# Kernel optimization log

Hardware: AMD Instinct MI355X
Metric: run time of the kernel (lower is better)

The kernel has to match this reference:

```python
import jax, jax.numpy as jnp
import numpy as np

B, N, M = 256, 50, 100
FSD, FVD, LDIM, BBD, INTER, K = 300, 2048, 2048, 128, 512, 8


def _linear(x, W, b):
    return x @ W + b


def bb_process(bb, W, b):
    # bb: [..., 4] = (x1, y1, x2, y2)
    size = bb[..., 2:] - bb[..., :2]
    centre = bb[..., :2] + 0.5 * size
    area = size[..., 0:1] * size[..., 1:2]
    shp = size[..., 0:1] / (size[..., 1:2] + 1e-14)
    feats = jnp.concatenate([bb, size, centre, area, shp], axis=-1)  # [..., 10]
    return _linear(feats, W, b)


def setup_inputs() -> dict:
    key = jax.random.key(0)
    ks = jax.random.split(key, 20)
    def nrm(k, shape, s=0.02):
        return jax.random.normal(k, shape, jnp.float32) * s
    # valid boxes: x2>x1, y2>y1
    xy_s = jax.random.uniform(ks[0], (B, N, 2)); wh_s = jax.random.uniform(ks[1], (B, N, 2))
    ps = jnp.concatenate([xy_s, xy_s + wh_s], -1)
    xy_v = jax.random.uniform(ks[2], (B, M, 2)); wh_v = jax.random.uniform(ks[3], (B, M, 2))
    pv = jnp.concatenate([xy_v, xy_v + wh_v], -1)
    return {
        "l": jax.random.normal(ks[4], (B, LDIM), jnp.float32),
        "s": jax.random.normal(ks[5], (B, N, FSD), jnp.float32),
        "ps": ps,
        "mask_s": jax.random.randint(ks[6], (B,), 1, N + 1),
        "v_ori": jax.random.normal(ks[7], (B, M, FVD), jnp.float32),
        "pv": pv,
        "mask_v": jnp.full((B,), M, dtype=jnp.int32),
        "W_bb": nrm(ks[8], (10, BBD)), "b_bb": jnp.zeros((BBD,), jnp.float32),
        "W1": nrm(ks[9], (K, BBD, INTER), 0.05),
        "W2": nrm(ks[10], (K, BBD, INTER), 0.05),
        "W_fs": nrm(ks[11], (FSD + BBD, FVD + BBD)), "b_fs": jnp.zeros((FVD + BBD,), jnp.float32),
        "W_l2": nrm(ks[12], (LDIM, FVD + BBD)), "b_l2": jnp.zeros((FVD + BBD,), jnp.float32),
        "W_l3": nrm(ks[13], (LDIM, FVD + BBD)), "b_l3": jnp.zeros((FVD + BBD,), jnp.float32),
        "W_fv": nrm(ks[14], (FVD + BBD, FVD + BBD)), "b_fv": jnp.zeros((FVD + BBD,), jnp.float32),
        "W_o1": nrm(ks[15], (BBD + FVD, FSD)), "b_o1": jnp.zeros((FSD,), jnp.float32),
        "W_o2": nrm(ks[16], (BBD + FVD, FVD)), "b_o2": jnp.zeros((FVD,), jnp.float32),
        "epsilon": jax.random.normal(ks[17], (), jnp.float32),
    }


def reference(l, s, ps, mask_s, v_ori, pv, mask_v,
              W_bb, b_bb, W1, W2, W_fs, b_fs, W_l2, b_l2, W_l3, b_l3,
              W_fv, b_fv, W_o1, b_o1, W_o2, b_o2, epsilon):
    # eval mode: no dropout, no cooling noise. it=1 (only valid setting), penalty_ratio=10.
    s_bb = bb_process(ps, W_bb, b_bb)            # [B,N,BBD]
    v_bb = bb_process(pv, W_bb, b_bb)            # [B,M,BBD]
    v = jnp.concatenate([v_ori, v_bb], -1)       # [B,M,FVD+BBD]
    lq = l[:, None, :]                           # [B,1,LDIM]
    token_mask = jnp.arange(N)[None, :] < mask_s[:, None]   # [B,N] bool
    out_mask = token_mask[:, :, None].astype(s.dtype)        # [B,N,1]
    # K-head bilinear adjacency over bounding-box embeddings
    s_f = jnp.einsum('bnd,kdi->bkni', s_bb, W1)  # [B,K,N,INTER]
    v_f = jnp.einsum('bmd,kdi->bkmi', v_bb, W2)  # [B,K,M,INTER]
    adj = jnp.einsum('bkni,bkmi->bnm', s_f, v_f) / K  # mean over heads
    adj = jax.nn.softmax(adj, axis=2)
    # cooling: pow(relu(adj), 1/0.25) then renormalize
    adj = jax.nn.relu(adj) ** 4.0
    adj = adj / jnp.sum(adj, axis=-1, keepdims=True)
    adj = adj * out_mask                          # [B,N,M]
    # gated message sources
    prepared_s = jax.nn.relu(_linear(
        _linear(jnp.concatenate([s, s_bb], -1), W_fs, b_fs) * _linear(lq, W_l3, b_l3),
        W_o2, b_o2))                              # [B,N,FVD]
    prepared_v = jax.nn.relu(_linear(
        _linear(v, W_fv, b_fv) * jax.nn.softmax(_linear(lq, W_l2, b_l2), axis=-1),
        W_o1, b_o1))                              # [B,M,FSD]
    # masked matmul aggregation
    new_ele = jnp.einsum('bnm,bnd->bmd', adj, prepared_s)   # [B,M,FVD]
    v_out = epsilon * new_ele + v_ori
    s_out = jnp.concatenate([s, jnp.einsum('bnm,bmd->bnd', adj, prepared_v)], -1)  # [B,N,2*FSD]
    adj_inf = jnp.where(token_mask[:, :, None], adj, -jnp.inf)  # adj + inf_tmp
    fro = jnp.sum(jnp.linalg.norm(adj, axis=-1), axis=-1) / mask_s.astype(jnp.float32)
    loss = -jnp.sum(fro) / 10.0                   # att_loss / penalty_ratio
    return (s_out * out_mask, v_out, adj_inf, loss)
```

## Files before the change

### kernel.cpp

```cpp
#include <hip/hip_runtime.h>
#include <math.h>

#define B_ 256
#define N_ 50
#define M_ 100
#define FSD_ 300
#define FVD_ 2048
#define LDIM_ 2048
#define BBD_ 128
#define INTER_ 512
#define K_ 8
#define DFS_ 428
#define DV_ 2176
#define NEGBIG_ (-3.0e38f)

typedef __attribute__((ext_vector_type(8))) short bf16x8_t;
typedef __attribute__((ext_vector_type(4))) float f32x4_t;

__device__ __forceinline__ unsigned short f2bf(float x) {
  union { float f; unsigned int u; } c; c.f = x;
  unsigned int r = c.u + 0x7FFFu + ((c.u >> 16) & 1u);
  return (unsigned short)(r >> 16);
}

__device__ __forceinline__ void gload16(const void* g, void* l) {
  __builtin_amdgcn_global_load_lds(
      (const __attribute__((address_space(1))) void*)g,
      (__attribute__((address_space(3))) void*)l, 16, 0, 0);
}

__global__ __launch_bounds__(128) void bb_kernel(const float* __restrict__ pbox,
                                                 const float* __restrict__ W_bb,
                                                 const float* __restrict__ b_bb,
                                                 float* __restrict__ outbb) {
  int row = blockIdx.x;
  int o = threadIdx.x;
  const float* p = pbox + (size_t)row * 4;
  float x0 = p[0], y0 = p[1], x1 = p[2], y1 = p[3];
  float sx = x1 - x0, sy = y1 - y0;
  float f[10] = {x0, y0, x1, y1, sx, sy, x0 + 0.5f * sx, y0 + 0.5f * sy,
                 sx * sy, sx / (sy + 1e-14f)};
  float acc = b_bb[o];
#pragma unroll
  for (int i = 0; i < 10; i++) acc += f[i] * W_bb[i * BBD_ + o];
  outbb[(size_t)row * BBD_ + o] = acc;
}

__global__ __launch_bounds__(128) void wq_kernel(const float* __restrict__ W1,
                                                 const float* __restrict__ W2,
                                                 float* __restrict__ Wq) {
  int d = blockIdx.x, e = threadIdx.x;
  __shared__ float w1row[INTER_];
  float acc = 0.f;
  for (int k = 0; k < K_; k++) {
    __syncthreads();
    for (int i = e; i < INTER_; i += 128) w1row[i] = W1[((size_t)k * BBD_ + d) * INTER_ + i];
    __syncthreads();
    const float* w2 = W2 + ((size_t)k * BBD_ + e) * INTER_;
#pragma unroll 8
    for (int i = 0; i < INTER_; i++) acc += w1row[i] * w2[i];
  }
  Wq[d * BBD_ + e] = acc * (1.0f / K_);
}

__global__ __launch_bounds__(128) void t_kernel(const float* __restrict__ s_bb,
                                                const float* __restrict__ Wq,
                                                float* __restrict__ t) {
  int row = blockIdx.x, e = threadIdx.x;
  __shared__ float srow[BBD_];
  srow[e] = s_bb[(size_t)row * BBD_ + e];
  __syncthreads();
  float acc = 0;
#pragma unroll 8
  for (int d = 0; d < BBD_; d++) acc += srow[d] * Wq[d * BBD_ + e];
  t[(size_t)row * BBD_ + e] = acc;
}

__global__ __launch_bounds__(128) void adjdot_kernel(const float* __restrict__ t,
                                                     const float* __restrict__ v_bb,
                                                     float* __restrict__ adjw) {
  int row = blockIdx.x;
  int b = row / N_;
  int tid = threadIdx.x;
  __shared__ float tS[BBD_];
  tS[tid] = t[(size_t)row * BBD_ + tid];
  __syncthreads();
  if (tid < M_) {
    const float4* vr = (const float4*)(v_bb + ((size_t)b * M_ + tid) * BBD_);
    const float4* tr = (const float4*)tS;
    float acc = 0.f;
#pragma unroll 8
    for (int d4 = 0; d4 < BBD_ / 4; d4++) {
      float4 vv = vr[d4];
      float4 tt = tr[d4];
      acc += tt.x * vv.x + tt.y * vv.y + tt.z * vv.z + tt.w * vv.w;
    }
    adjw[(size_t)row * M_ + tid] = acc * 4.0f;
  }
}

__global__ __launch_bounds__(64) void adjsm_kernel(float* __restrict__ adjw,
                                                   const int* __restrict__ mask_s,
                                                   float* __restrict__ adj_inf,
                                                   float* __restrict__ lossbuf) {
  int row = blockIdx.x;
  int b = row / N_, n = row % N_;
  int tid = threadIdx.x;
  float* xr = adjw + (size_t)row * M_;
  int i1 = tid + 64;
  float v0 = xr[tid];
  float v1 = (i1 < M_) ? xr[i1] : -INFINITY;
  float mx = fmaxf(v0, v1);
#pragma unroll
  for (int off = 32; off > 0; off >>= 1) mx = fmaxf(mx, __shfl_xor(mx, off));
  float e0 = __expf(v0 - mx);
  float e1 = (i1 < M_) ? __expf(v1 - mx) : 0.f;
  float sm = e0 + e1;
#pragma unroll
  for (int off = 32; off > 0; off >>= 1) sm += __shfl_xor(sm, off);
  float inv = 1.0f / sm;
  int msk = mask_s[b];
  bool live = n < msk;
  float a0 = live ? e0 * inv : 0.f;
  float a1 = live ? e1 * inv : 0.f;
  xr[tid] = a0;
  adj_inf[(size_t)row * M_ + tid] = live ? a0 : NEGBIG_;
  if (i1 < M_) {
    xr[i1] = a1;
    adj_inf[(size_t)row * M_ + i1] = live ? a1 : NEGBIG_;
  }
  float n2 = a0 * a0 + a1 * a1;
#pragma unroll
  for (int off = 32; off > 0; off >>= 1) n2 += __shfl_xor(n2, off);
  if (tid == 0) lossbuf[row] = sqrtf(n2) / (float)msk;
}

__global__ __launch_bounds__(256) void lossred_kernel(const float* __restrict__ lossbuf,
                                                      float* __restrict__ loss) {
  int tid = threadIdx.x;
  float s = 0;
  for (int i = tid; i < B_ * N_; i += 256) s += lossbuf[i];
  __shared__ float red[4];
#pragma unroll
  for (int off = 32; off > 0; off >>= 1) s += __shfl_xor(s, off);
  if ((tid & 63) == 0) red[tid >> 6] = s;
  __syncthreads();
  if (tid == 0) loss[0] = -(red[0] + red[1] + red[2] + red[3]) / 10.0f;
}

__global__ __launch_bounds__(256) void softmax_kernel(float* __restrict__ g) {
  __shared__ float buf[DV_];
  __shared__ float red[4];
  __shared__ float bc;
  int b = blockIdx.x, tid = threadIdx.x;
  float* row = g + (size_t)b * DV_;
  float mx = -INFINITY;
  for (int i = tid; i < DV_; i += 256) {
    float v = row[i];
    buf[i] = v;
    mx = fmaxf(mx, v);
  }
#pragma unroll
  for (int off = 32; off > 0; off >>= 1) mx = fmaxf(mx, __shfl_xor(mx, off));
  if ((tid & 63) == 0) red[tid >> 6] = mx;
  __syncthreads();
  if (tid == 0) bc = fmaxf(fmaxf(red[0], red[1]), fmaxf(red[2], red[3]));
  __syncthreads();
  mx = bc;
  float sm = 0;
  for (int i = tid; i < DV_; i += 256) {
    float e = __expf(buf[i] - mx);
    buf[i] = e;
    sm += e;
  }
#pragma unroll
  for (int off = 32; off > 0; off >>= 1) sm += __shfl_xor(sm, off);
  if ((tid & 63) == 0) red[tid >> 6] = sm;
  __syncthreads();
  if (tid == 0) bc = red[0] + red[1] + red[2] + red[3];
  __syncthreads();
  float inv = 1.0f / bc;
  for (int i = tid; i < DV_; i += 256) row[i] = buf[i] * inv;
}

__global__ __launch_bounds__(256) void wtrans_kernel(const float* __restrict__ W,
                                                     unsigned short* __restrict__ Wt,
                                                     int K, int N, int Kpad) {
  __shared__ float tile[32][33];
  int n0 = blockIdx.x * 32, k0 = blockIdx.y * 32;
  int tj = threadIdx.x & 31, ti0 = threadIdx.x >> 5;
#pragma unroll
  for (int s = 0; s < 4; ++s) {
    int ki = k0 + ti0 + s * 8;
    int nj = n0 + tj;
    tile[ti0 + s * 8][tj] = (ki < K && nj < N) ? W[(size_t)ki * N + nj] : 0.f;
  }
  __syncthreads();
#pragma unroll
  for (int s = 0; s < 4; ++s) {
    int nloc = ti0 + s * 8;
    Wt[(size_t)(n0 + nloc) * Kpad + k0 + tj] = f2bf(tile[tj][nloc]);
  }
}

__global__ __launch_bounds__(256) void cat2bf_kernel(const float* __restrict__ A0, int ca,
                                                     const float* __restrict__ A1, int cb,
                                                     unsigned short* __restrict__ dst,
                                                     int cpad) {
  int row = blockIdx.y;
  int c4 = (blockIdx.x * 256 + threadIdx.x) * 4;
  if (c4 >= cpad) return;
  float4 v = make_float4(0.f, 0.f, 0.f, 0.f);
  if (c4 < ca)
    v = *(const float4*)(A0 + (size_t)row * ca + c4);
  else if (c4 < ca + cb)
    v = *(const float4*)(A1 + (size_t)row * cb + (c4 - ca));
  unsigned long long p = (unsigned long long)f2bf(v.x) |
                         ((unsigned long long)f2bf(v.y) << 16) |
                         ((unsigned long long)f2bf(v.z) << 32) |
                         ((unsigned long long)f2bf(v.w) << 48);
  *(unsigned long long*)(dst + (size_t)row * cpad + c4) = p;
}

template <int EPI, bool OBF>
__global__ __launch_bounds__(256) void mfma_gemm(
    const unsigned short* __restrict__ A, const unsigned short* __restrict__ Bt,
    const float* __restrict__ bias, const float* __restrict__ gate,
    void* __restrict__ Cout, int Kpad, int Ncols, int NStore, int ldc, int rows_per_b) {
  __shared__ unsigned short As[128 * 64];
  __shared__ unsigned short Bs[128 * 64];
  int tid = threadIdx.x;
  int wid = tid >> 6, lane = tid & 63;
  int wm = wid >> 1, wn = wid & 1;
  int lr = lane & 15, lh = lane >> 4;
  int row0 = blockIdx.y * 128, col0 = blockIdx.x * 128;

  f32x4_t acc[4][4];
#pragma unroll
  for (int m = 0; m < 4; ++m)
#pragma unroll
    for (int n = 0; n < 4; ++n) acc[m][n] = (f32x4_t){0.f, 0.f, 0.f, 0.f};

  int sr[4], sj[4];
#pragma unroll
  for (int c = 0; c < 4; ++c) {
    int b = ((c * 4 + wid) << 10) + lane * 16;
    sr[c] = b >> 7;
    sj[c] = ((b & 127) ^ ((sr[c] & 7) << 4)) >> 1;
  }

  int nK = Kpad >> 6;
  for (int kt = 0; kt < nK; ++kt) {
    int k0 = kt << 6;
#pragma unroll
    for (int c = 0; c < 4; ++c) {
      gload16(A + (size_t)(row0 + sr[c]) * Kpad + k0 + sj[c], &As[(c * 4 + wid) << 9]);
      gload16(Bt + (size_t)(col0 + sr[c]) * Kpad + k0 + sj[c], &Bs[(c * 4 + wid) << 9]);
    }
    __syncthreads();
    bf16x8_t af[4][2], bfr[4][2];
#pragma unroll
    for (int m = 0; m < 4; ++m) {
      int rl = wm * 64 + m * 16 + lr;
      int sw = (rl & 7) << 4;
#pragma unroll
      for (int kk = 0; kk < 2; ++kk) {
        int inner = ((kk * 64 + lh * 16) ^ sw) >> 1;
        af[m][kk] = *(const bf16x8_t*)&As[rl * 64 + inner];
      }
    }
#pragma unroll
    for (int n = 0; n < 4; ++n) {
      int nl = wn * 64 + n * 16 + lr;
      int sw = (nl & 7) << 4;
#pragma unroll
      for (int kk = 0; kk < 2; ++kk) {
        int inner = ((kk * 64 + lh * 16) ^ sw) >> 1;
        bfr[n][kk] = *(const bf16x8_t*)&Bs[nl * 64 + inner];
      }
    }
#pragma unroll
    for (int m = 0; m < 4; ++m)
#pragma unroll
      for (int n = 0; n < 4; ++n) {
        acc[m][n] = __builtin_amdgcn_mfma_f32_16x16x32_bf16(af[m][0], bfr[n][0], acc[m][n], 0, 0, 0);
        acc[m][n] = __builtin_amdgcn_mfma_f32_16x16x32_bf16(af[m][1], bfr[n][1], acc[m][n], 0, 0, 0);
      }
    __syncthreads();
  }

#pragma unroll
  for (int m = 0; m < 4; ++m) {
    int gr0 = row0 + wm * 64 + m * 16 + lh * 4;
#pragma unroll
    for (int n = 0; n < 4; ++n) {
      int gc = col0 + wn * 64 + n * 16 + lr;
      if (gc >= NStore) continue;
      float bv = bias[gc];
      f32x4_t v = acc[m][n];
#pragma unroll
      for (int i = 0; i < 4; ++i) {
        int gr = gr0 + i;
        float x = v[i] + bv;
        if constexpr (EPI == 1) x *= gate[(size_t)(gr / rows_per_b) * Ncols + gc];
        if constexpr (EPI == 2) x = fmaxf(x, 0.f);
        if constexpr (OBF)
          ((unsigned short*)Cout)[(size_t)gr * ldc + gc] = f2bf(x);
        else
          ((float*)Cout)[(size_t)gr * ldc + gc] = x;
      }
    }
  }
}

__global__ __launch_bounds__(128) void outv_kernel(const float* __restrict__ adjw,
                                                   const float* __restrict__ ps_prep,
                                                   const float* __restrict__ v_ori,
                                                   const float* __restrict__ eps_p,
                                                   float* __restrict__ v_out) {
  int b = blockIdx.x;
  int ch = blockIdx.y;
  int tid = threadIdx.x;
  __shared__ float psc[N_][128];
  __shared__ float adjs[N_ * M_];
  for (int i = tid; i < N_ * 128; i += 128) {
    int n = i >> 7, c = i & 127;
    psc[n][c] = ps_prep[((size_t)b * N_ + n) * FVD_ + ch * 128 + c];
  }
  for (int i = tid; i < N_ * M_; i += 128) adjs[i] = adjw[(size_t)b * N_ * M_ + i];
  __syncthreads();
  float eps = eps_p[0];
  int col4 = (tid & 31) * 4;
  int mbase = (tid >> 5) * 25;
  for (int mb = 0; mb < 25; mb += 5) {
    f32x4_t acc[5];
#pragma unroll
    for (int q = 0; q < 5; ++q) acc[q] = (f32x4_t){0.f, 0.f, 0.f, 0.f};
    const float* arow = adjs + mbase + mb;
#pragma unroll 2
    for (int n = 0; n < N_; ++n) {
      f32x4_t p = *(const f32x4_t*)&psc[n][col4];
#pragma unroll
      for (int q = 0; q < 5; ++q) acc[q] += arow[n * M_ + q] * p;
    }
#pragma unroll
    for (int q = 0; q < 5; ++q) {
      int m = mbase + mb + q;
      size_t base = ((size_t)b * M_ + m) * FVD_ + ch * 128 + col4;
      f32x4_t vo = *(const f32x4_t*)&v_ori[base];
      *(f32x4_t*)&v_out[base] = eps * acc[q] + vo;
    }
  }
}

__global__ __launch_bounds__(256) void outs_kernel(const float* __restrict__ s,
                                                   const float* __restrict__ adjw,
                                                   const float* __restrict__ pv_prep,
                                                   const int* __restrict__ mask_s,
                                                   float* __restrict__ s_out) {
  int b = blockIdx.x;
  int c0 = blockIdx.y * 64;
  int tid = threadIdx.x;
  __shared__ float pvc[M_ * 64];
  __shared__ float adjs[52 * M_];
  for (int i = tid; i < M_ * 64; i += 256) {
    int m = i >> 6, c = c0 + (i & 63);
    pvc[i] = (c < FSD_) ? pv_prep[((size_t)b * M_ + m) * FSD_ + c] : 0.f;
  }
  for (int i = tid; i < 52 * M_; i += 256)
    adjs[i] = (i < N_ * M_) ? adjw[(size_t)b * N_ * M_ + i] : 0.f;
  __syncthreads();
  int col = tid & 63, ngrp = tid >> 6;
  int msk = mask_s[b];
  float acc[13];
#pragma unroll
  for (int i = 0; i < 13; ++i) acc[i] = 0.f;
  for (int m = 0; m < M_; ++m) {
    float pv = pvc[m * 64 + col];
#pragma unroll
    for (int i = 0; i < 13; ++i) acc[i] += adjs[(ngrp * 13 + i) * M_ + m] * pv;
  }
  int gc = c0 + col;
  if (gc < FSD_) {
#pragma unroll
    for (int i = 0; i < 13; ++i) {
      int n = ngrp * 13 + i;
      if (n >= N_) break;
      size_t row = (size_t)b * N_ + n;
      bool live = n < msk;
      s_out[row * (2 * FSD_) + gc] = live ? s[row * FSD_ + gc] : 0.f;
      s_out[row * (2 * FSD_) + FSD_ + gc] = acc[i];
    }
  }
}

extern "C" void kernel_launch(void* const* d_in, const int* in_sizes, int n_in,
                              void* d_out, int out_size, void* d_ws, size_t ws_size,
                              hipStream_t stream) {
  (void)in_sizes; (void)n_in; (void)out_size; (void)ws_size;
  const float* l = (const float*)d_in[0];
  const float* s = (const float*)d_in[1];
  const float* ps_box = (const float*)d_in[2];
  const int* mask_s = (const int*)d_in[3];
  const float* v_ori = (const float*)d_in[4];
  const float* pv_box = (const float*)d_in[5];
  const float* W_bb = (const float*)d_in[7];
  const float* b_bb = (const float*)d_in[8];
  const float* W1 = (const float*)d_in[9];
  const float* W2 = (const float*)d_in[10];
  const float* W_fs = (const float*)d_in[11];
  const float* b_fs = (const float*)d_in[12];
  const float* W_l2 = (const float*)d_in[13];
  const float* b_l2 = (const float*)d_in[14];
  const float* W_l3 = (const float*)d_in[15];
  const float* b_l3 = (const float*)d_in[16];
  const float* W_fv = (const float*)d_in[17];
  const float* b_fv = (const float*)d_in[18];
  const float* W_o1 = (const float*)d_in[19];
  const float* b_o1 = (const float*)d_in[20];
  const float* W_o2 = (const float*)d_in[21];
  const float* b_o2 = (const float*)d_in[22];
  const float* eps = (const float*)d_in[23];

  float* ws = (float*)d_ws;
  float* s_bb = ws;
  float* v_bb = s_bb + 1638400;
  float* Wq = v_bb + 3276800;
  float* t = Wq + 16384;
  float* adjw = t + 1638400;
  float* lossbuf = adjw + 1280000;
  float* g3 = lossbuf + 12800;
  float* g2 = g3 + 557056;
  float* ps_prep = g2 + 557056;
  float* pv_prep = ps_prep + 26214400;
  unsigned short* bfb = (unsigned short*)(pv_prep + 7680000);
  unsigned short* R1 = bfb;
  unsigned short* R2 = R1 + 55705600;
  unsigned short* Wt_fs = R2 + 55705600;
  unsigned short* Wt_o2 = Wt_fs + 974848;
  unsigned short* Wt_fv = Wt_o2 + 4456448;
  unsigned short* Wt_o1 = Wt_fv + 4734976;
  unsigned short* Wt_l2 = Wt_o1 + 835584;
  unsigned short* Wt_l3 = Wt_l2 + 4456448;
  unsigned short* A_l = Wt_l3 + 4456448;
  unsigned short* A_fv = R1;
  unsigned short* A_fs = R1;
  unsigned short* h_bf = R1 + 8000000;
  unsigned short* y_bf = R2;

  float* out = (float*)d_out;
  float* o_sout = out;
  float* o_vout = out + 7680000;
  float* o_adjinf = out + 60108800;
  float* o_loss = out + 61388800;

  bb_kernel<<<B_ * N_, 128, 0, stream>>>(ps_box, W_bb, b_bb, s_bb);
  bb_kernel<<<B_ * M_, 128, 0, stream>>>(pv_box, W_bb, b_bb, v_bb);
  wq_kernel<<<BBD_, 128, 0, stream>>>(W1, W2, Wq);
  t_kernel<<<B_ * N_, 128, 0, stream>>>(s_bb, Wq, t);
  adjdot_kernel<<<B_ * N_, 128, 0, stream>>>(t, v_bb, adjw);
  adjsm_kernel<<<B_ * N_, 64, 0, stream>>>(adjw, mask_s, o_adjinf, lossbuf);
  lossred_kernel<<<1, 256, 0, stream>>>(lossbuf, o_loss);

  wtrans_kernel<<<dim3(68, 64), 256, 0, stream>>>(W_l3, Wt_l3, LDIM_, DV_, 2048);
  wtrans_kernel<<<dim3(68, 64), 256, 0, stream>>>(W_l2, Wt_l2, LDIM_, DV_, 2048);
  wtrans_kernel<<<dim3(68, 68), 256, 0, stream>>>(W_fv, Wt_fv, DV_, DV_, 2176);
  wtrans_kernel<<<dim3(12, 68), 256, 0, stream>>>(W_o1, Wt_o1, DV_, FSD_, 2176);
  wtrans_kernel<<<dim3(68, 14), 256, 0, stream>>>(W_fs, Wt_fs, DFS_, DV_, 448);
  wtrans_kernel<<<dim3(64, 68), 256, 0, stream>>>(W_o2, Wt_o2, DV_, FVD_, 2176);
  cat2bf_kernel<<<dim3(2, B_), 256, 0, stream>>>(l, LDIM_, nullptr, 0, A_l, 2048);

  mfma_gemm<0, false><<<dim3(17, 2), 256, 0, stream>>>(A_l, Wt_l3, b_l3, nullptr, g3,
                                                       2048, DV_, DV_, DV_, 1);
  mfma_gemm<0, false><<<dim3(17, 2), 256, 0, stream>>>(A_l, Wt_l2, b_l2, nullptr, g2,
                                                       2048, DV_, DV_, DV_, 1);
  softmax_kernel<<<B_, 256, 0, stream>>>(g2);

  cat2bf_kernel<<<dim3(3, B_ * M_), 256, 0, stream>>>(v_ori, FVD_, v_bb, BBD_, A_fv, 2176);
  mfma_gemm<1, true><<<dim3(17, 200), 256, 0, stream>>>(A_fv, Wt_fv, b_fv, g2, y_bf,
                                                        2176, DV_, DV_, DV_, M_);
  mfma_gemm<2, false><<<dim3(3, 200), 256, 0, stream>>>(y_bf, Wt_o1, b_o1, nullptr, pv_prep,
                                                        2176, DV_, FSD_, FSD_, 1);

  cat2bf_kernel<<<dim3(1, B_ * N_), 256, 0, stream>>>(s, FSD_, s_bb, BBD_, A_fs, 448);
  mfma_gemm<1, true><<<dim3(17, 100), 256, 0, stream>>>(A_fs, Wt_fs, b_fs, g3, h_bf,
                                                        448, DV_, DV_, DV_, N_);
  mfma_gemm<2, false><<<dim3(16, 100), 256, 0, stream>>>(h_bf, Wt_o2, b_o2, nullptr, ps_prep,
                                                         2176, FVD_, FVD_, FVD_, 1);

  outv_kernel<<<dim3(B_, 16), 128, 0, stream>>>(adjw, ps_prep, v_ori, eps, o_vout);
  outs_kernel<<<dim3(B_, 5), 256, 0, stream>>>(s, adjw, pv_prep, mask_s, o_sout);
}
```

Measured before the change: 1.792 ms.

## Double-buffer GEMM LDS tiles, remap workgroups across XCDs, merge query GEMMs

The MFMA GEMM now uses two LDS buffers so the global loads for the next K tile are issued while the current tile is computed, which halves the barriers per tile. Workgroup IDs are remapped so that consecutive tiles land on the same XCD for better L2 locality. The two small query GEMMs (W_l3 and W_l2) are merged into one launch over concatenated weights and biases, with strided softmax and gate reads. Doubling LDS to 64KB per block may reduce occupancy.

Result: no change. 1.767 ms (-1.4%).

```diff
diff --git a/kernel.cpp b/kernel.cpp
--- a/kernel.cpp
+++ b/kernel.cpp
@@ -148,12 +148,12 @@
   if (tid == 0) loss[0] = -(red[0] + red[1] + red[2] + red[3]) / 10.0f;
 }
 
-__global__ __launch_bounds__(256) void softmax_kernel(float* __restrict__ g) {
+__global__ __launch_bounds__(256) void softmax_kernel(float* __restrict__ g, int ld) {
   __shared__ float buf[DV_];
   __shared__ float red[4];
   __shared__ float bc;
   int b = blockIdx.x, tid = threadIdx.x;
-  float* row = g + (size_t)b * DV_;
+  float* row = g + (size_t)b * ld;
   float mx = -INFINITY;
   for (int i = tid; i < DV_; i += 256) {
     float v = row[i];
@@ -222,18 +222,36 @@
   *(unsigned long long*)(dst + (size_t)row * cpad + c4) = p;
 }
 
+__global__ __launch_bounds__(256) void catbias_kernel(const float* __restrict__ a,
+                                                      const float* __restrict__ b,
+                                                      float* __restrict__ dst) {
+  int i = blockIdx.x * 256 + threadIdx.x;
+  if (i < DV_) {
+    dst[i] = a[i];
+    dst[DV_ + i] = b[i];
+  }
+}
+
 template <int EPI, bool OBF>
 __global__ __launch_bounds__(256) void mfma_gemm(
     const unsigned short* __restrict__ A, const unsigned short* __restrict__ Bt,
     const float* __restrict__ bias, const float* __restrict__ gate,
-    void* __restrict__ Cout, int Kpad, int Ncols, int NStore, int ldc, int rows_per_b) {
-  __shared__ unsigned short As[128 * 64];
-  __shared__ unsigned short Bs[128 * 64];
+    void* __restrict__ Cout, int Klen, int lda, int ldb, int gate_ld,
+    int NStore, int ldc, int rows_per_b) {
+  __shared__ unsigned short As[2][128 * 64];
+  __shared__ unsigned short Bs[2][128 * 64];
   int tid = threadIdx.x;
   int wid = tid >> 6, lane = tid & 63;
   int wm = wid >> 1, wn = wid & 1;
   int lr = lane & 15, lh = lane >> 4;
-  int row0 = blockIdx.y * 128, col0 = blockIdx.x * 128;
+
+  int nwg = gridDim.x * gridDim.y;
+  int orig = blockIdx.y * gridDim.x + blockIdx.x;
+  int q = nwg >> 3, r = nwg & 7;
+  int xcd = orig & 7, idx = orig >> 3;
+  int wgid = (xcd < r ? xcd * (q + 1) : r * (q + 1) + (xcd - r) * q) + idx;
+  int row0 = (wgid / gridDim.x) * 128;
+  int col0 = (wgid % gridDim.x) * 128;
 
   f32x4_t acc[4][4];
 #pragma unroll
@@ -249,15 +267,16 @@
     sj[c] = ((b & 127) ^ ((sr[c] & 7) << 4)) >> 1;
   }
 
-  int nK = Kpad >> 6;
-  for (int kt = 0; kt < nK; ++kt) {
+  auto STAGE = [&](int buf, int kt) {
     int k0 = kt << 6;
 #pragma unroll
     for (int c = 0; c < 4; ++c) {
-      gload16(A + (size_t)(row0 + sr[c]) * Kpad + k0 + sj[c], &As[(c * 4 + wid) << 9]);
-      gload16(Bt + (size_t)(col0 + sr[c]) * Kpad + k0 + sj[c], &Bs[(c * 4 + wid) << 9]);
-    }
-    __syncthreads();
+      gload16(A + (size_t)(row0 + sr[c]) * lda + k0 + sj[c], &As[buf][(c * 4 + wid) << 9]);
+      gload16(Bt + (size_t)(col0 + sr[c]) * ldb + k0 + sj[c], &Bs[buf][(c * 4 + wid) << 9]);
+    }
+  };
+
+  auto COMPUTE = [&](const unsigned short* as, const unsigned short* bs) {
     bf16x8_t af[4][2], bfr[4][2];
 #pragma unroll
     for (int m = 0; m < 4; ++m) {
@@ -266,7 +285,7 @@
 #pragma unroll
       for (int kk = 0; kk < 2; ++kk) {
         int inner = ((kk * 64 + lh * 16) ^ sw) >> 1;
-        af[m][kk] = *(const bf16x8_t*)&As[rl * 64 + inner];
+        af[m][kk] = *(const bf16x8_t*)&as[rl * 64 + inner];
       }
     }
 #pragma unroll
@@ -276,7 +295,7 @@
 #pragma unroll
       for (int kk = 0; kk < 2; ++kk) {
         int inner = ((kk * 64 + lh * 16) ^ sw) >> 1;
-        bfr[n][kk] = *(const bf16x8_t*)&Bs[nl * 64 + inner];
+        bfr[n][kk] = *(const bf16x8_t*)&bs[nl * 64 + inner];
       }
     }
 #pragma unroll
@@ -286,7 +305,20 @@
         acc[m][n] = __builtin_amdgcn_mfma_f32_16x16x32_bf16(af[m][0], bfr[n][0], acc[m][n], 0, 0, 0);
         acc[m][n] = __builtin_amdgcn_mfma_f32_16x16x32_bf16(af[m][1], bfr[n][1], acc[m][n], 0, 0, 0);
       }
+  };
+
+  int nK = Klen >> 6;
+  STAGE(0, 0);
+  __syncthreads();
+  for (int kt = 0; kt < nK; kt += 2) {
+    if (kt + 1 < nK) STAGE(1, kt + 1);
+    COMPUTE(&As[0][0], &Bs[0][0]);
     __syncthreads();
+    if (kt + 1 < nK) {
+      if (kt + 2 < nK) STAGE(0, kt + 2);
+      COMPUTE(&As[1][0], &Bs[1][0]);
+      __syncthreads();
+    }
   }
 
 #pragma unroll
@@ -302,7 +334,7 @@
       for (int i = 0; i < 4; ++i) {
         int gr = gr0 + i;
         float x = v[i] + bv;
-        if constexpr (EPI == 1) x *= gate[(size_t)(gr / rows_per_b) * Ncols + gc];
+        if constexpr (EPI == 1) x *= gate[(size_t)(gr / rows_per_b) * gate_ld + gc];
         if constexpr (EPI == 2) x = fmaxf(x, 0.f);
         if constexpr (OBF)
           ((unsigned short*)Cout)[(size_t)gr * ldc + gc] = f2bf(x);
@@ -429,9 +461,8 @@
   float* t = Wq + 16384;
   float* adjw = t + 1638400;
   float* lossbuf = adjw + 1280000;
-  float* g3 = lossbuf + 12800;
-  float* g2 = g3 + 557056;
-  float* ps_prep = g2 + 557056;
+  float* g_all = lossbuf + 12800;
+  float* ps_prep = g_all + 1114112;
   float* pv_prep = ps_prep + 26214400;
   unsigned short* bfb = (unsigned short*)(pv_prep + 7680000);
   unsigned short* R1 = bfb;
@@ -440,13 +471,15 @@
   unsigned short* Wt_o2 = Wt_fs + 974848;
   unsigned short* Wt_fv = Wt_o2 + 4456448;
   unsigned short* Wt_o1 = Wt_fv + 4734976;
-  unsigned short* Wt_l2 = Wt_o1 + 835584;
-  unsigned short* Wt_l3 = Wt_l2 + 4456448;
-  unsigned short* A_l = Wt_l3 + 4456448;
+  unsigned short* Wt_l23 = Wt_o1 + 835584;
+  unsigned short* A_l = Wt_l23 + 8912896;
+  float* b_l23 = (float*)(A_l + 524288);
   unsigned short* A_fv = R1;
   unsigned short* A_fs = R1;
   unsigned short* h_bf = R1 + 8000000;
   unsigned short* y_bf = R2;
+  float* g3v = g_all;
+  float* g2v = g_all + DV_;
 
   float* out = (float*)d_out;
   float* o_sout = out;
@@ -462,31 +495,30 @@
   adjsm_kernel<<<B_ * N_, 64, 0, stream>>>(adjw, mask_s, o_adjinf, lossbuf);
   lossred_kernel<<<1, 256, 0, stream>>>(lossbuf, o_loss);
 
-  wtrans_kernel<<<dim3(68, 64), 256, 0, stream>>>(W_l3, Wt_l3, LDIM_, DV_, 2048);
-  wtrans_kernel<<<dim3(68, 64), 256, 0, stream>>>(W_l2, Wt_l2, LDIM_, DV_, 2048);
+  wtrans_kernel<<<dim3(68, 64), 256, 0, stream>>>(W_l3, Wt_l23, LDIM_, DV_, 2048);
+  wtrans_kernel<<<dim3(68, 64), 256, 0, stream>>>(W_l2, Wt_l23 + (size_t)DV_ * 2048, LDIM_, DV_, 2048);
   wtrans_kernel<<<dim3(68, 68), 256, 0, stream>>>(W_fv, Wt_fv, DV_, DV_, 2176);
   wtrans_kernel<<<dim3(12, 68), 256, 0, stream>>>(W_o1, Wt_o1, DV_, FSD_, 2176);
   wtrans_kernel<<<dim3(68, 14), 256, 0, stream>>>(W_fs, Wt_fs, DFS_, DV_, 448);
   wtrans_kernel<<<dim3(64, 68), 256, 0, stream>>>(W_o2, Wt_o2, DV_, FVD_, 2176);
   cat2bf_kernel<<<dim3(2, B_), 256, 0, stream>>>(l, LDIM_, nullptr, 0, A_l, 2048);
-
-  mfma_gemm<0, false><<<dim3(17, 2), 256, 0, stream>>>(A_l, Wt_l3, b_l3, nullptr, g3,
-                                                       2048, DV_, DV_, DV_, 1);
-  mfma_gemm<0, false><<<dim3(17, 2), 256, 0, stream>>>(A_l, Wt_l2, b_l2, nullptr, g2,
-                                                       2048, DV_, DV_, DV_, 1);
-  softmax_kernel<<<B_, 256, 0, stream>>>(g2);
+  catbias_kernel<<<9, 256, 0, stream>>>(b_l3, b_l2, b_l23);
+
+  mfma_gemm<0, false><<<dim3(34, 2), 256, 0, stream>>>(
+      A_l, Wt_l23, b_l23, nullptr, g_all, 2048, 2048, 2048, 0, 4352, 4352, 1);
+  softmax_kernel<<<B_, 256, 0, stream>>>(g2v, 4352);
 
   cat2bf_kernel<<<dim3(3, B_ * M_), 256, 0, stream>>>(v_ori, FVD_, v_bb, BBD_, A_fv, 2176);
-  mfma_gemm<1, true><<<dim3(17, 200), 256, 0, stream>>>(A_fv, Wt_fv, b_fv, g2, y_bf,
-                                                        2176, DV_, DV_, DV_, M_);
-  mfma_gemm<2, false><<<dim3(3, 200), 256, 0, stream>>>(y_bf, Wt_o1, b_o1, nullptr, pv_prep,
-                                                        2176, DV_, FSD_, FSD_, 1);
+  mfma_gemm<1, true><<<dim3(17, 200), 256, 0, stream>>>(
+      A_fv, Wt_fv, b_fv, g2v, y_bf, 2176, 2176, 2176, 4352, DV_, DV_, M_);
+  mfma_gemm<2, false><<<dim3(3, 200), 256, 0, stream>>>(
+      y_bf, Wt_o1, b_o1, nullptr, pv_prep, 2176, 2176, 2176, 0, FSD_, FSD_, 1);
 
   cat2bf_kernel<<<dim3(1, B_ * N_), 256, 0, stream>>>(s, FSD_, s_bb, BBD_, A_fs, 448);
-  mfma_gemm<1, true><<<dim3(17, 100), 256, 0, stream>>>(A_fs, Wt_fs, b_fs, g3, h_bf,
-                                                        448, DV_, DV_, DV_, N_);
-  mfma_gemm<2, false><<<dim3(16, 100), 256, 0, stream>>>(h_bf, Wt_o2, b_o2, nullptr, ps_prep,
-                                                         2176, FVD_, FVD_, FVD_, 1);
+  mfma_gemm<1, true><<<dim3(17, 100), 256, 0, stream>>>(
+      A_fs, Wt_fs, b_fs, g3v, h_bf, 448, 448, 448, 4352, DV_, DV_, N_);
+  mfma_gemm<2, false><<<dim3(16, 100), 256, 0, stream>>>(
+      h_bf, Wt_o2, b_o2, nullptr, ps_prep, 2176, 2176, 2176, 0, FVD_, FVD_, 1);
 
   outv_kernel<<<dim3(B_, 16), 128, 0, stream>>>(adjw, ps_prep, v_ori, eps, o_vout);
   outs_kernel<<<dim3(B_, 5), 256, 0, stream>>>(s, adjw, pv_prep, mask_s, o_sout);
```
